# Kernel tuning notes

Hardware: AMD Instinct MI355X
Metric: run time of the kernel (lower is better)

## Reference

```python
import jax, jax.numpy as jnp
import numpy as np

B, CIN, COUT, N, M, K = 8, 128, 256, 8192, 2048, 16
BN_EPS = 1e-5


def setup_inputs() -> dict:
    key = jax.random.key(0)
    k1, k2, k3 = jax.random.split(key, 3)
    x = jax.random.normal(k1, (B, CIN, N), dtype=jnp.float32)
    coords = jax.random.normal(k2, (B, 3, N), dtype=jnp.float32)
    W = jax.random.normal(k3, (COUT, CIN), dtype=jnp.float32) * 0.05  # 1x1 conv, bias=False
    gamma = jnp.ones((COUT,), dtype=jnp.float32)   # BatchNorm2d weight
    beta = jnp.zeros((COUT,), dtype=jnp.float32)   # BatchNorm2d bias
    return {"x": x, "coords": coords, "W": W, "gamma": gamma, "beta": beta}


def furthest_point_sampling(coords, num_samples):
    """coords: (B,3,N) -> indices (B,num_samples) int32. Greedy FPS starting at index 0."""
    pts = coords.transpose(0, 2, 1)  # (B,N,3)
    b, n, _ = pts.shape
    idx0 = jnp.zeros((b,), dtype=jnp.int32)
    mind0 = jnp.full((b, n), 1e10, dtype=pts.dtype)

    def step(carry, _):
        mind, last = carry
        lastpt = jnp.take_along_axis(pts, last[:, None, None], axis=1)  # (b,1,3)
        d = jnp.sum((pts - lastpt) ** 2, axis=-1)                        # (b,n)
        mind = jnp.minimum(mind, d)
        nxt = jnp.argmax(mind, axis=-1).astype(jnp.int32)
        return (mind, nxt), nxt

    (_, _), rest = jax.lax.scan(step, (mind0, idx0), None, length=num_samples - 1)
    return jnp.concatenate([idx0[:, None], rest.T], axis=1)  # (b,num_samples)


def reference(x, coords, W, gamma, beta):
    b = x.shape[0]
    fps_idx = furthest_point_sampling(coords, M)                # (B,M)
    pts = coords.transpose(0, 2, 1)                             # (B,N,3)
    bidx = jnp.arange(b)[:, None]
    fps_pts = pts[bidx, fps_idx]                                # (B,M,3)

    # squared-distance matrix via ||a||^2 + ||b||^2 - 2ab (avoids (B,M,N,3) temp)
    d = (jnp.sum(fps_pts ** 2, -1)[:, :, None]
         + jnp.sum(pts ** 2, -1)[:, None, :]
         - 2.0 * jnp.einsum('bmd,bnd->bmn', fps_pts, pts))      # (B,M,N)
    _, knn_idx = jax.lax.top_k(-d, K)                           # (B,M,K) nearest (sorted)

    x_t = x.transpose(0, 2, 1)                                  # (B,N,Cin)
    knn = x_t[jnp.arange(b)[:, None, None], knn_idx]            # (B,M,K,Cin)

    # PointwiseConv2D: 1x1 conv (no bias) + BatchNorm2d (batch stats) + ReLU
    h = jnp.einsum('bmkc,oc->bmko', knn, W)                     # (B,M,K,Cout)
    mean = jnp.mean(h, axis=(0, 1, 2))
    var = jnp.var(h, axis=(0, 1, 2))
    h = (h - mean) * jax.lax.rsqrt(var + BN_EPS) * gamma + beta
    h = jax.nn.relu(h)

    y = jnp.max(h, axis=2).transpose(0, 2, 1)                   # (B,Cout,M), max over k
    fps_coords = fps_pts.transpose(0, 2, 1)                     # (B,3,M)
    return y, fps_coords
```

## Files before the change

kernel.cpp:

```cpp
#include <hip/hip_runtime.h>
#include <math.h>

#define B_ 8
#define CIN_ 128
#define COUT_ 256
#define N_ 8192
#define M_ 2048
#define K_ 16

__device__ __forceinline__ unsigned umax2(unsigned a, unsigned b) { return a > b ? a : b; }
__device__ __forceinline__ unsigned umin2(unsigned a, unsigned b) { return a < b ? a : b; }

__device__ __forceinline__ unsigned wave_reduce_umax(unsigned v) {
    v = umax2(v, (unsigned)__builtin_amdgcn_update_dpp(0, (int)v, 0x111, 0xf, 0xf, false));
    v = umax2(v, (unsigned)__builtin_amdgcn_update_dpp(0, (int)v, 0x112, 0xf, 0xf, false));
    v = umax2(v, (unsigned)__builtin_amdgcn_update_dpp(0, (int)v, 0x114, 0xf, 0xf, false));
    v = umax2(v, (unsigned)__builtin_amdgcn_update_dpp(0, (int)v, 0x118, 0xf, 0xf, false));
    v = umax2(v, (unsigned)__builtin_amdgcn_update_dpp(0, (int)v, 0x142, 0xf, 0xf, false));
    v = umax2(v, (unsigned)__builtin_amdgcn_update_dpp(0, (int)v, 0x143, 0xf, 0xf, false));
    return (unsigned)__builtin_amdgcn_readlane((int)v, 63);
}
__device__ __forceinline__ unsigned wave_reduce_umin(unsigned v) {
    v = umin2(v, (unsigned)__builtin_amdgcn_update_dpp(-1, (int)v, 0x111, 0xf, 0xf, false));
    v = umin2(v, (unsigned)__builtin_amdgcn_update_dpp(-1, (int)v, 0x112, 0xf, 0xf, false));
    v = umin2(v, (unsigned)__builtin_amdgcn_update_dpp(-1, (int)v, 0x114, 0xf, 0xf, false));
    v = umin2(v, (unsigned)__builtin_amdgcn_update_dpp(-1, (int)v, 0x118, 0xf, 0xf, false));
    v = umin2(v, (unsigned)__builtin_amdgcn_update_dpp(-1, (int)v, 0x142, 0xf, 0xf, false));
    v = umin2(v, (unsigned)__builtin_amdgcn_update_dpp(-1, (int)v, 0x143, 0xf, 0xf, false));
    return (unsigned)__builtin_amdgcn_readlane((int)v, 63);
}

__global__ __launch_bounds__(512) void fps_kernel(const float* __restrict__ coords,
                                                  float* __restrict__ fpts,
                                                  float* __restrict__ out_fps) {
#pragma clang fp contract(off)
    const int b = blockIdx.x;
    const int tid = threadIdx.x;
    const int lane = tid & 63;
    const int wid = tid >> 6;
    const float* cb = coords + (size_t)b * 3 * N_;

    __shared__ float4 pts[N_];
    __shared__ __align__(16) unsigned long long kbuf[2][8];
    __shared__ int wlist[M_];

    float px[16], py[16], pz[16], mind[16];
#pragma unroll
    for (int s = 0; s < 16; ++s) {
        int p = tid + s * 512;
        px[s] = cb[p];
        py[s] = cb[N_ + p];
        pz[s] = cb[2 * N_ + p];
        mind[s] = 1e10f;
        pts[p] = make_float4(px[s], py[s], pz[s], 0.f);
    }
    __syncthreads();
    float4 p0 = pts[0];
    float lx = p0.x, ly = p0.y, lz = p0.z;

    int par = 0;
    for (int m = 1; m < M_; ++m) {
        float bv = -1.0f; int bs = 0;
#pragma unroll
        for (int s = 0; s < 16; ++s) {
            float dx = px[s] - lx;
            float dy = py[s] - ly;
            float dz = pz[s] - lz;
            float d = __builtin_fmaf(dz, dz, __builtin_fmaf(dy, dy, dx * dx));
            float mn = fminf(mind[s], d);
            mind[s] = mn;
            if (mn > bv) { bv = mn; bs = s; }
        }
        int bi = tid + bs * 512;
        unsigned kd = __float_as_uint(bv);
        unsigned md = wave_reduce_umax(kd);
        unsigned cand = (kd == md) ? (unsigned)bi : 0xffffffffu;
        unsigned mi = wave_reduce_umin(cand);
        if (lane == 0)
            kbuf[par][wid] = ((unsigned long long)md << 32) |
                             (unsigned long long)(0xffffffffu - mi);
        __syncthreads();
        const unsigned long long* kb = kbuf[par];
        ulonglong2 q0 = *(const ulonglong2*)&kb[0];
        ulonglong2 q1 = *(const ulonglong2*)&kb[2];
        ulonglong2 q2 = *(const ulonglong2*)&kb[4];
        ulonglong2 q3 = *(const ulonglong2*)&kb[6];
        unsigned long long a0 = q0.x > q0.y ? q0.x : q0.y;
        unsigned long long a1 = q1.x > q1.y ? q1.x : q1.y;
        unsigned long long a2 = q2.x > q2.y ? q2.x : q2.y;
        unsigned long long a3 = q3.x > q3.y ? q3.x : q3.y;
        unsigned long long b01 = a0 > a1 ? a0 : a1;
        unsigned long long b23 = a2 > a3 ? a2 : a3;
        unsigned long long best = b01 > b23 ? b01 : b23;
        int widx = (int)(0xffffffffu - (unsigned)(best & 0xffffffffull));
        widx = ((unsigned)widx < (unsigned)N_) ? widx : 0;
        float4 wp = pts[widx];
        lx = wp.x; ly = wp.y; lz = wp.z;
        if (tid == 0) wlist[m] = widx;
        par ^= 1;
    }

    __syncthreads();
    for (int mm = tid; mm < M_; mm += 512) {
        int wi = (mm == 0) ? 0 : wlist[mm];
        wi = ((unsigned)wi < (unsigned)N_) ? wi : 0;
        float4 wp = pts[wi];
        ((float4*)fpts)[b * M_ + mm] = make_float4(wp.x, wp.y, wp.z, 0.f);
        out_fps[(size_t)b * 3 * M_ + 0 * M_ + mm] = wp.x;
        out_fps[(size_t)b * 3 * M_ + 1 * M_ + mm] = wp.y;
        out_fps[(size_t)b * 3 * M_ + 2 * M_ + mm] = wp.z;
    }
}

__global__ __launch_bounds__(256) void knn_kernel(const float* __restrict__ coords,
                                                  const float* __restrict__ fpts,
                                                  int* __restrict__ knn) {
#pragma clang fp contract(off)
    const int bidx = blockIdx.x;
    const int b = bidx >> 9;
    const int mg = bidx & 511;
    const int tid = threadIdx.x;
    const int lane = tid & 63;
    const int w = tid >> 6;
    const int m = mg * 4 + w;
    const int row = b * M_ + m;
    const float* cb = coords + (size_t)b * 3 * N_;

    __shared__ float4 tile[1024];

    float4 f = ((const float4*)fpts)[row];
    const float fx = f.x, fy = f.y, fz = f.z;
    const float sf = __builtin_fmaf(fz, fz, __builtin_fmaf(fy, fy, fx * fx));

    float ed = INFINITY; int ei = 0x7fffffff;
    float tau_d = INFINITY; int tau_i = 0x7fffffff;

    for (int t = 0; t < 8; ++t) {
        const int base = t * 1024;
#pragma unroll
        for (int j = 0; j < 4; ++j) {
            int idx = tid + 256 * j;
            int n = base + idx;
            float gx = cb[n], gy = cb[N_ + n], gz = cb[2 * N_ + n];
            float sp = __builtin_fmaf(gz, gz, __builtin_fmaf(gy, gy, gx * gx));
            tile[idx] = make_float4(gx, gy, gz, sp);
        }
        __syncthreads();
        for (int s = 0; s < 16; ++s) {
            int l = s * 64 + lane;
            float4 p = tile[l];
            int n = base + l;
            float dot = __builtin_fmaf(fz, p.z, __builtin_fmaf(fy, p.y, fx * p.x));
            float d = (sf + p.w) - 2.0f * dot;
            bool q = (d < tau_d) || (d == tau_d && n < tau_i);
            unsigned long long bal = __ballot(q);
            while (bal) {
                int lb = __ffsll(bal) - 1;
                bal &= bal - 1;
                float dv = __shfl(d, lb);
                int   iv = __shfl(n, lb);
                if ((dv < tau_d) || (dv == tau_d && iv < tau_i)) {
                    float pud = __shfl_up(ed, 1);
                    int   pui = __shfl_up(ei, 1);
                    bool cs = (dv < ed) || (dv == ed && iv < ei);
                    bool cp = (lane != 0) && ((dv < pud) || (dv == pud && iv < pui));
                    ed = cs ? (cp ? pud : dv) : ed;
                    ei = cs ? (cp ? pui : iv) : ei;
                    tau_d = __shfl(ed, 15);
                    tau_i = __shfl(ei, 15);
                }
            }
        }
        __syncthreads();
    }
    if (lane < K_) {
        int v = ei;
        knn[(size_t)row * K_ + lane] = ((unsigned)v < (unsigned)N_) ? v : 0;
    }
}

__global__ __launch_bounds__(256) void gemm_kernel(const float* __restrict__ x,
                                                   const float* __restrict__ W,
                                                   float* __restrict__ hp) {
    const int bid = blockIdx.x;
    const int b = bid >> 9;
    const int rem = bid & 511;
    const int n0 = (rem >> 2) * 64;
    const int o0 = (rem & 3) * 64;
    const int tid = threadIdx.x;
    const int tn = (tid & 15) * 4;
    const int to = (tid >> 4) * 4;
    const float* xg = x + (size_t)b * CIN_ * N_;

    __shared__ float Xs[64][64];
    __shared__ float Wt[64][68];

    float acc[4][4] = {};
    for (int kk = 0; kk < CIN_; kk += 64) {
#pragma unroll
        for (int i = 0; i < 16; ++i) {
            int e = tid + 256 * i;
            int r = e >> 6, q = e & 63;
            Xs[r][q] = xg[(size_t)(kk + r) * N_ + n0 + q];
            Wt[q][r] = W[(size_t)(o0 + r) * CIN_ + kk + q];
        }
        __syncthreads();
#pragma unroll 8
        for (int c = 0; c < 64; ++c) {
            float4 a = *(const float4*)&Xs[c][tn];
            float4 bb = *(const float4*)&Wt[c][to];
            float av[4] = {a.x, a.y, a.z, a.w};
            float bv[4] = {bb.x, bb.y, bb.z, bb.w};
#pragma unroll
            for (int j = 0; j < 4; ++j)
#pragma unroll
                for (int l = 0; l < 4; ++l)
                    acc[j][l] += av[j] * bv[l];
        }
        __syncthreads();
    }
#pragma unroll
    for (int j = 0; j < 4; ++j) {
        float4 v = make_float4(acc[j][0], acc[j][1], acc[j][2], acc[j][3]);
        *(float4*)&hp[((size_t)b * N_ + n0 + tn + j) * COUT_ + o0 + to] = v;
    }
}

__global__ __launch_bounds__(256) void stats_partial_kernel(const float* __restrict__ hp,
                                                            const int* __restrict__ knn,
                                                            double* __restrict__ partial,
                                                            double* __restrict__ partial2) {
    const int o = threadIdx.x;
    const int g0 = blockIdx.x * 1024;
    double s = 0.0, s2 = 0.0;
    for (int r = 0; r < 1024; ++r) {
        int g = g0 + r;
        int row = g >> 4;
        int k = g & 15;
        int b = row >> 11;
        int n = knn[row * K_ + k];
        n = ((unsigned)n < (unsigned)N_) ? n : 0;
        double h = (double)hp[((size_t)b * N_ + n) * COUT_ + o];
        s += h;
        s2 += h * h;
    }
    partial[(size_t)blockIdx.x * 256 + o] = s;
    partial2[(size_t)blockIdx.x * 256 + o] = s2;
}

__global__ void bn_final_kernel(const double* __restrict__ partial,
                                const double* __restrict__ partial2,
                                const float* __restrict__ gamma,
                                const float* __restrict__ beta,
                                float* __restrict__ scale,
                                float* __restrict__ bias) {
    int o = threadIdx.x;
    double s = 0.0, s2 = 0.0;
    for (int j = 0; j < 256; ++j) {
        s += partial[(size_t)j * 256 + o];
        s2 += partial2[(size_t)j * 256 + o];
    }
    const double inv = 1.0 / (double)(B_ * M_ * K_);
    double mean = s * inv;
    double var = s2 * inv - mean * mean;
    if (var < 0.0) var = 0.0;
    double r = 1.0 / sqrt(var + 1e-5);
    double g = (double)gamma[o];
    scale[o] = (float)(r * g);
    bias[o] = (float)((double)beta[o] - mean * r * g);
}

__global__ __launch_bounds__(256) void finalize_kernel(const float* __restrict__ hp,
                                                       const int* __restrict__ knn,
                                                       const float* __restrict__ scale,
                                                       const float* __restrict__ bias,
                                                       float* __restrict__ y) {
    const int b = blockIdx.x >> 6;
    const int m0 = (blockIdx.x & 63) * 32;
    const int tid = threadIdx.x;
    __shared__ int kidx[512];
    __shared__ float tile[32][257];

    for (int e = tid; e < 512; e += 256) {
        int n = knn[(b * M_ + m0 + (e >> 4)) * K_ + (e & 15)];
        kidx[e] = ((unsigned)n < (unsigned)N_) ? n : 0;
    }
    __syncthreads();

    const float s = scale[tid];
    const float t = bias[tid];
    const float* hb = hp + (size_t)b * N_ * COUT_;
    for (int mm = 0; mm < 32; ++mm) {
        float v = -INFINITY;
#pragma unroll
        for (int k = 0; k < K_; ++k) {
            int n = kidx[mm * 16 + k];
            float h = hb[(size_t)n * COUT_ + tid];
            v = fmaxf(v, h * s + t);
        }
        v = fmaxf(v, 0.0f);
        tile[mm][tid] = v;
    }
    __syncthreads();
#pragma unroll
    for (int r = 0; r < 32; ++r) {
        int o2 = r * 8 + (tid >> 5);
        int mm = tid & 31;
        y[((size_t)b * COUT_ + o2) * M_ + m0 + mm] = tile[mm][o2];
    }
}

__global__ void sentinel_kernel(float* out, float v) { out[0] = v; }

extern "C" void kernel_launch(void* const* d_in, const int* in_sizes, int n_in,
                              void* d_out, int out_size, void* d_ws, size_t ws_size,
                              hipStream_t stream) {
    const float* x = (const float*)d_in[0];
    const float* coords = (const float*)d_in[1];
    const float* W = (const float*)d_in[2];
    const float* gamma = (const float*)d_in[3];
    const float* beta = (const float*)d_in[4];
    float* y = (float*)d_out;
    float* out_fps = y + (size_t)B_ * COUT_ * M_;

    if (n_in != 5 ||
        in_sizes[0] != B_ * CIN_ * N_ ||
        in_sizes[1] != B_ * 3 * N_ ||
        in_sizes[2] != COUT_ * CIN_ ||
        in_sizes[3] != COUT_ || in_sizes[4] != COUT_ ||
        out_size != B_ * COUT_ * M_ + B_ * 3 * M_) {
        sentinel_kernel<<<1, 1, 0, stream>>>(y, -2.0e6f);
        return;
    }

    const size_t HP_BYTES = (size_t)B_ * N_ * COUT_ * 4;
    const size_t FPTS_BYTES = (size_t)B_ * M_ * 16;
    const size_t KNN_BYTES = (size_t)B_ * M_ * K_ * 4;
    const size_t PART_BYTES = (size_t)256 * 256 * 8;
    const size_t NEED = HP_BYTES + FPTS_BYTES + KNN_BYTES + 2 * PART_BYTES + 8192;
    if (ws_size < NEED) {
        sentinel_kernel<<<1, 1, 0, stream>>>(y, -1.0e6f);
        return;
    }
    char* ws = (char*)d_ws;
    float* hp = (float*)ws;
    float* fpts = (float*)(ws + HP_BYTES);
    int* knn = (int*)(ws + HP_BYTES + FPTS_BYTES);
    double* partial = (double*)(ws + HP_BYTES + FPTS_BYTES + KNN_BYTES);
    double* partial2 = (double*)(ws + HP_BYTES + FPTS_BYTES + KNN_BYTES + PART_BYTES);
    float* scale = (float*)(ws + HP_BYTES + FPTS_BYTES + KNN_BYTES + 2 * PART_BYTES);
    float* bias = scale + 256;

    fps_kernel<<<B_, 512, 0, stream>>>(coords, fpts, out_fps);
    knn_kernel<<<B_ * 512, 256, 0, stream>>>(coords, fpts, knn);
    gemm_kernel<<<B_ * 512, 256, 0, stream>>>(x, W, hp);
    stats_partial_kernel<<<256, 256, 0, stream>>>(hp, knn, partial, partial2);
    bn_final_kernel<<<1, 256, 0, stream>>>(partial, partial2, gamma, beta, scale, bias);
    finalize_kernel<<<512, 256, 0, stream>>>(hp, knn, scale, bias, y);
}
```

Baseline: 1.954 ms.

## Shrink FPS block to 256 threads and fuse argmax into a single 64-bit DPP reduction

The FPS kernel now runs 256 threads, each holding 32 points in registers instead of 16, so each barrier-synchronised iteration involves 4 waves instead of 8. The two-pass wave reduction (max of the distance, then min of the index) is replaced by one DPP reduction on a packed (distance, inverted index) 64-bit key, which shortens the serial critical path of each of the 2047 steps. The cost is twice the per-thread serial distance work and higher register pressure (launch_bounds 256,1).

```diff
diff --git a/kernel.cpp b/kernel.cpp
--- a/kernel.cpp
+++ b/kernel.cpp
@@ -8,31 +8,16 @@
 #define M_ 2048
 #define K_ 16
 
-__device__ __forceinline__ unsigned umax2(unsigned a, unsigned b) { return a > b ? a : b; }
-__device__ __forceinline__ unsigned umin2(unsigned a, unsigned b) { return a < b ? a : b; }
-
-__device__ __forceinline__ unsigned wave_reduce_umax(unsigned v) {
-    v = umax2(v, (unsigned)__builtin_amdgcn_update_dpp(0, (int)v, 0x111, 0xf, 0xf, false));
-    v = umax2(v, (unsigned)__builtin_amdgcn_update_dpp(0, (int)v, 0x112, 0xf, 0xf, false));
-    v = umax2(v, (unsigned)__builtin_amdgcn_update_dpp(0, (int)v, 0x114, 0xf, 0xf, false));
-    v = umax2(v, (unsigned)__builtin_amdgcn_update_dpp(0, (int)v, 0x118, 0xf, 0xf, false));
-    v = umax2(v, (unsigned)__builtin_amdgcn_update_dpp(0, (int)v, 0x142, 0xf, 0xf, false));
-    v = umax2(v, (unsigned)__builtin_amdgcn_update_dpp(0, (int)v, 0x143, 0xf, 0xf, false));
-    return (unsigned)__builtin_amdgcn_readlane((int)v, 63);
-}
-__device__ __forceinline__ unsigned wave_reduce_umin(unsigned v) {
-    v = umin2(v, (unsigned)__builtin_amdgcn_update_dpp(-1, (int)v, 0x111, 0xf, 0xf, false));
-    v = umin2(v, (unsigned)__builtin_amdgcn_update_dpp(-1, (int)v, 0x112, 0xf, 0xf, false));
-    v = umin2(v, (unsigned)__builtin_amdgcn_update_dpp(-1, (int)v, 0x114, 0xf, 0xf, false));
-    v = umin2(v, (unsigned)__builtin_amdgcn_update_dpp(-1, (int)v, 0x118, 0xf, 0xf, false));
-    v = umin2(v, (unsigned)__builtin_amdgcn_update_dpp(-1, (int)v, 0x142, 0xf, 0xf, false));
-    v = umin2(v, (unsigned)__builtin_amdgcn_update_dpp(-1, (int)v, 0x143, 0xf, 0xf, false));
-    return (unsigned)__builtin_amdgcn_readlane((int)v, 63);
-}
-
-__global__ __launch_bounds__(512) void fps_kernel(const float* __restrict__ coords,
-                                                  float* __restrict__ fpts,
-                                                  float* __restrict__ out_fps) {
+#define KSTEP(CTL) {                                                                     \
+    unsigned h2 = (unsigned)__builtin_amdgcn_update_dpp(0, (int)hi, CTL, 0xf, 0xf, false); \
+    unsigned l2 = (unsigned)__builtin_amdgcn_update_dpp(0, (int)lo, CTL, 0xf, 0xf, false); \
+    unsigned long long cur = ((unsigned long long)hi << 32) | lo;                        \
+    unsigned long long oth = ((unsigned long long)h2 << 32) | l2;                        \
+    if (oth > cur) { hi = h2; lo = l2; } }
+
+__global__ __launch_bounds__(256, 1) void fps_kernel(const float* __restrict__ coords,
+                                                     float* __restrict__ fpts,
+                                                     float* __restrict__ out_fps) {
 #pragma clang fp contract(off)
     const int b = blockIdx.x;
     const int tid = threadIdx.x;
@@ -41,13 +26,13 @@
     const float* cb = coords + (size_t)b * 3 * N_;
 
     __shared__ float4 pts[N_];
-    __shared__ __align__(16) unsigned long long kbuf[2][8];
+    __shared__ __align__(16) unsigned long long kbuf[2][4];
     __shared__ int wlist[M_];
 
-    float px[16], py[16], pz[16], mind[16];
-#pragma unroll
-    for (int s = 0; s < 16; ++s) {
-        int p = tid + s * 512;
+    float px[32], py[32], pz[32], mind[32];
+#pragma unroll
+    for (int s = 0; s < 32; ++s) {
+        int p = tid + s * 256;
         px[s] = cb[p];
         py[s] = cb[N_ + p];
         pz[s] = cb[2 * N_ + p];
@@ -62,7 +47,7 @@
     for (int m = 1; m < M_; ++m) {
         float bv = -1.0f; int bs = 0;
 #pragma unroll
-        for (int s = 0; s < 16; ++s) {
+        for (int s = 0; s < 32; ++s) {
             float dx = px[s] - lx;
             float dy = py[s] - ly;
             float dz = pz[s] - lz;
@@ -71,27 +56,22 @@
             mind[s] = mn;
             if (mn > bv) { bv = mn; bs = s; }
         }
-        int bi = tid + bs * 512;
-        unsigned kd = __float_as_uint(bv);
-        unsigned md = wave_reduce_umax(kd);
-        unsigned cand = (kd == md) ? (unsigned)bi : 0xffffffffu;
-        unsigned mi = wave_reduce_umin(cand);
-        if (lane == 0)
-            kbuf[par][wid] = ((unsigned long long)md << 32) |
-                             (unsigned long long)(0xffffffffu - mi);
-        __syncthreads();
-        const unsigned long long* kb = kbuf[par];
-        ulonglong2 q0 = *(const ulonglong2*)&kb[0];
-        ulonglong2 q1 = *(const ulonglong2*)&kb[2];
-        ulonglong2 q2 = *(const ulonglong2*)&kb[4];
-        ulonglong2 q3 = *(const ulonglong2*)&kb[6];
+        unsigned hi = __float_as_uint(bv);
+        unsigned lo = 0xffffffffu - (unsigned)(tid + bs * 256);
+        KSTEP(0x111)
+        KSTEP(0x112)
+        KSTEP(0x114)
+        KSTEP(0x118)
+        KSTEP(0x142)
+        KSTEP(0x143)
+        if (lane == 63)
+            kbuf[par][wid] = ((unsigned long long)hi << 32) | (unsigned long long)lo;
+        __syncthreads();
+        ulonglong2 q0 = *(const ulonglong2*)&kbuf[par][0];
+        ulonglong2 q1 = *(const ulonglong2*)&kbuf[par][2];
         unsigned long long a0 = q0.x > q0.y ? q0.x : q0.y;
         unsigned long long a1 = q1.x > q1.y ? q1.x : q1.y;
-        unsigned long long a2 = q2.x > q2.y ? q2.x : q2.y;
-        unsigned long long a3 = q3.x > q3.y ? q3.x : q3.y;
-        unsigned long long b01 = a0 > a1 ? a0 : a1;
-        unsigned long long b23 = a2 > a3 ? a2 : a3;
-        unsigned long long best = b01 > b23 ? b01 : b23;
+        unsigned long long best = a0 > a1 ? a0 : a1;
         int widx = (int)(0xffffffffu - (unsigned)(best & 0xffffffffull));
         widx = ((unsigned)widx < (unsigned)N_) ? widx : 0;
         float4 wp = pts[widx];
@@ -101,7 +81,7 @@
     }
 
     __syncthreads();
-    for (int mm = tid; mm < M_; mm += 512) {
+    for (int mm = tid; mm < M_; mm += 256) {
         int wi = (mm == 0) ? 0 : wlist[mm];
         wi = ((unsigned)wi < (unsigned)N_) ? wi : 0;
         float4 wp = pts[wi];
@@ -351,7 +331,7 @@
     float* scale = (float*)(ws + HP_BYTES + FPTS_BYTES + KNN_BYTES + 2 * PART_BYTES);
     float* bias = scale + 256;
 
-    fps_kernel<<<B_, 512, 0, stream>>>(coords, fpts, out_fps);
+    fps_kernel<<<B_, 256, 0, stream>>>(coords, fpts, out_fps);
     knn_kernel<<<B_ * 512, 256, 0, stream>>>(coords, fpts, knn);
     gemm_kernel<<<B_ * 512, 256, 0, stream>>>(x, W, hp);
     stats_partial_kernel<<<256, 256, 0, stream>>>(hp, knn, partial, partial2);
```

Result: slower. 2.325 ms (+19.0%).

## Fuse FPS and pointwise GEMM into one launch so GEMM overlaps FPS

Applied to the files above, without the earlier changes.

FPS and the input GEMM now run in a single kernel. The first 8 blocks do the serial furthest-point sampling, and the remaining 2048 blocks compute the GEMM with 512-thread, 128-wide tiles. Shared memory is a union of the two layouts. The goal is to hide the GEMM inside the long, low-occupancy FPS phase, which runs on only 8 blocks. In exchange, every block reserves the large FPS shared-memory footprint, which limits GEMM occupancy, and the GEMM tile shape changes.

```diff
diff --git a/kernel.cpp b/kernel.cpp
--- a/kernel.cpp
+++ b/kernel.cpp
@@ -7,6 +7,8 @@
 #define N_ 8192
 #define M_ 2048
 #define K_ 16
+
+#define GEMM_BLOCKS 2048
 
 __device__ __forceinline__ unsigned umax2(unsigned a, unsigned b) { return a > b ? a : b; }
 __device__ __forceinline__ unsigned umin2(unsigned a, unsigned b) { return a < b ? a : b; }
@@ -30,85 +32,148 @@
     return (unsigned)__builtin_amdgcn_readlane((int)v, 63);
 }
 
-__global__ __launch_bounds__(512) void fps_kernel(const float* __restrict__ coords,
-                                                  float* __restrict__ fpts,
-                                                  float* __restrict__ out_fps) {
+__global__ __launch_bounds__(512) void fps_gemm_kernel(const float* __restrict__ coords,
+                                                       const float* __restrict__ x,
+                                                       const float* __restrict__ W,
+                                                       float* __restrict__ fpts,
+                                                       float* __restrict__ out_fps,
+                                                       float* __restrict__ hp) {
+    __shared__ union {
+        struct {
+            float4 pts[N_];
+            unsigned long long kbuf[2][8];
+            int wlist[M_];
+        } f;
+        struct {
+            float Xs[64][128];
+            float Wt[64][68];
+        } g;
+    } sm;
+
+    const int tid = threadIdx.x;
+
+    if (blockIdx.x < B_) {
 #pragma clang fp contract(off)
-    const int b = blockIdx.x;
-    const int tid = threadIdx.x;
-    const int lane = tid & 63;
-    const int wid = tid >> 6;
-    const float* cb = coords + (size_t)b * 3 * N_;
-
-    __shared__ float4 pts[N_];
-    __shared__ __align__(16) unsigned long long kbuf[2][8];
-    __shared__ int wlist[M_];
-
-    float px[16], py[16], pz[16], mind[16];
-#pragma unroll
-    for (int s = 0; s < 16; ++s) {
-        int p = tid + s * 512;
-        px[s] = cb[p];
-        py[s] = cb[N_ + p];
-        pz[s] = cb[2 * N_ + p];
-        mind[s] = 1e10f;
-        pts[p] = make_float4(px[s], py[s], pz[s], 0.f);
-    }
-    __syncthreads();
-    float4 p0 = pts[0];
-    float lx = p0.x, ly = p0.y, lz = p0.z;
-
-    int par = 0;
-    for (int m = 1; m < M_; ++m) {
-        float bv = -1.0f; int bs = 0;
+        const int b = blockIdx.x;
+        const int lane = tid & 63;
+        const int wid = tid >> 6;
+        const float* cb = coords + (size_t)b * 3 * N_;
+        float4* pts = sm.f.pts;
+        unsigned long long (*kbuf)[8] = sm.f.kbuf;
+        int* wlist = sm.f.wlist;
+
+        float px[16], py[16], pz[16], mind[16];
 #pragma unroll
         for (int s = 0; s < 16; ++s) {
-            float dx = px[s] - lx;
-            float dy = py[s] - ly;
-            float dz = pz[s] - lz;
-            float d = __builtin_fmaf(dz, dz, __builtin_fmaf(dy, dy, dx * dx));
-            float mn = fminf(mind[s], d);
-            mind[s] = mn;
-            if (mn > bv) { bv = mn; bs = s; }
-        }
-        int bi = tid + bs * 512;
-        unsigned kd = __float_as_uint(bv);
-        unsigned md = wave_reduce_umax(kd);
-        unsigned cand = (kd == md) ? (unsigned)bi : 0xffffffffu;
-        unsigned mi = wave_reduce_umin(cand);
-        if (lane == 0)
-            kbuf[par][wid] = ((unsigned long long)md << 32) |
-                             (unsigned long long)(0xffffffffu - mi);
+            int p = tid + s * 512;
+            px[s] = cb[p];
+            py[s] = cb[N_ + p];
+            pz[s] = cb[2 * N_ + p];
+            mind[s] = 1e10f;
+            pts[p] = make_float4(px[s], py[s], pz[s], 0.f);
+        }
         __syncthreads();
-        const unsigned long long* kb = kbuf[par];
-        ulonglong2 q0 = *(const ulonglong2*)&kb[0];
-        ulonglong2 q1 = *(const ulonglong2*)&kb[2];
-        ulonglong2 q2 = *(const ulonglong2*)&kb[4];
-        ulonglong2 q3 = *(const ulonglong2*)&kb[6];
-        unsigned long long a0 = q0.x > q0.y ? q0.x : q0.y;
-        unsigned long long a1 = q1.x > q1.y ? q1.x : q1.y;
-        unsigned long long a2 = q2.x > q2.y ? q2.x : q2.y;
-        unsigned long long a3 = q3.x > q3.y ? q3.x : q3.y;
-        unsigned long long b01 = a0 > a1 ? a0 : a1;
-        unsigned long long b23 = a2 > a3 ? a2 : a3;
-        unsigned long long best = b01 > b23 ? b01 : b23;
-        int widx = (int)(0xffffffffu - (unsigned)(best & 0xffffffffull));
-        widx = ((unsigned)widx < (unsigned)N_) ? widx : 0;
-        float4 wp = pts[widx];
-        lx = wp.x; ly = wp.y; lz = wp.z;
-        if (tid == 0) wlist[m] = widx;
-        par ^= 1;
-    }
-
-    __syncthreads();
-    for (int mm = tid; mm < M_; mm += 512) {
-        int wi = (mm == 0) ? 0 : wlist[mm];
-        wi = ((unsigned)wi < (unsigned)N_) ? wi : 0;
-        float4 wp = pts[wi];
-        ((float4*)fpts)[b * M_ + mm] = make_float4(wp.x, wp.y, wp.z, 0.f);
-        out_fps[(size_t)b * 3 * M_ + 0 * M_ + mm] = wp.x;
-        out_fps[(size_t)b * 3 * M_ + 1 * M_ + mm] = wp.y;
-        out_fps[(size_t)b * 3 * M_ + 2 * M_ + mm] = wp.z;
+        float4 p0 = pts[0];
+        float lx = p0.x, ly = p0.y, lz = p0.z;
+
+        int par = 0;
+        for (int m = 1; m < M_; ++m) {
+            float bv = -1.0f; int bs = 0;
+#pragma unroll
+            for (int s = 0; s < 16; ++s) {
+                float dx = px[s] - lx;
+                float dy = py[s] - ly;
+                float dz = pz[s] - lz;
+                float d = __builtin_fmaf(dz, dz, __builtin_fmaf(dy, dy, dx * dx));
+                float mn = fminf(mind[s], d);
+                mind[s] = mn;
+                if (mn > bv) { bv = mn; bs = s; }
+            }
+            int bi = tid + bs * 512;
+            unsigned kd = __float_as_uint(bv);
+            unsigned md = wave_reduce_umax(kd);
+            unsigned cand = (kd == md) ? (unsigned)bi : 0xffffffffu;
+            unsigned mi = wave_reduce_umin(cand);
+            if (lane == 0)
+                kbuf[par][wid] = ((unsigned long long)md << 32) |
+                                 (unsigned long long)(0xffffffffu - mi);
+            __syncthreads();
+            const unsigned long long* kb = kbuf[par];
+            ulonglong2 q0 = *(const ulonglong2*)&kb[0];
+            ulonglong2 q1 = *(const ulonglong2*)&kb[2];
+            ulonglong2 q2 = *(const ulonglong2*)&kb[4];
+            ulonglong2 q3 = *(const ulonglong2*)&kb[6];
+            unsigned long long a0 = q0.x > q0.y ? q0.x : q0.y;
+            unsigned long long a1 = q1.x > q1.y ? q1.x : q1.y;
+            unsigned long long a2 = q2.x > q2.y ? q2.x : q2.y;
+            unsigned long long a3 = q3.x > q3.y ? q3.x : q3.y;
+            unsigned long long b01 = a0 > a1 ? a0 : a1;
+            unsigned long long b23 = a2 > a3 ? a2 : a3;
+            unsigned long long best = b01 > b23 ? b01 : b23;
+            int widx = (int)(0xffffffffu - (unsigned)(best & 0xffffffffull));
+            widx = ((unsigned)widx < (unsigned)N_) ? widx : 0;
+            float4 wp = pts[widx];
+            lx = wp.x; ly = wp.y; lz = wp.z;
+            if (tid == 0) wlist[m] = widx;
+            par ^= 1;
+        }
+
+        __syncthreads();
+        for (int mm = tid; mm < M_; mm += 512) {
+            int wi = (mm == 0) ? 0 : wlist[mm];
+            wi = ((unsigned)wi < (unsigned)N_) ? wi : 0;
+            float4 wp = pts[wi];
+            ((float4*)fpts)[b * M_ + mm] = make_float4(wp.x, wp.y, wp.z, 0.f);
+            out_fps[(size_t)b * 3 * M_ + 0 * M_ + mm] = wp.x;
+            out_fps[(size_t)b * 3 * M_ + 1 * M_ + mm] = wp.y;
+            out_fps[(size_t)b * 3 * M_ + 2 * M_ + mm] = wp.z;
+        }
+    } else {
+        const int gb = blockIdx.x - B_;
+        const int b = gb >> 8;
+        const int rem = gb & 255;
+        const int n0 = (rem >> 2) * 128;
+        const int o0 = (rem & 3) * 64;
+        const int tn = (tid & 31) * 4;
+        const int to = (tid >> 5) * 4;
+        const float* xg = x + (size_t)b * CIN_ * N_;
+        float (*Xs)[128] = sm.g.Xs;
+        float (*Wt)[68] = sm.g.Wt;
+
+        float acc[4][4] = {};
+        for (int kk = 0; kk < CIN_; kk += 64) {
+#pragma unroll
+            for (int i = 0; i < 16; ++i) {
+                int e = tid + 512 * i;
+                int r = e >> 7, q = e & 127;
+                Xs[r][q] = xg[(size_t)(kk + r) * N_ + n0 + q];
+            }
+#pragma unroll
+            for (int i = 0; i < 8; ++i) {
+                int e = tid + 512 * i;
+                int r = e >> 6, q = e & 63;
+                Wt[q][r] = W[(size_t)(o0 + r) * CIN_ + kk + q];
+            }
+            __syncthreads();
+#pragma unroll 8
+            for (int c = 0; c < 64; ++c) {
+                float4 a = *(const float4*)&Xs[c][tn];
+                float4 bb = *(const float4*)&Wt[c][to];
+                float av[4] = {a.x, a.y, a.z, a.w};
+                float bv[4] = {bb.x, bb.y, bb.z, bb.w};
+#pragma unroll
+                for (int j = 0; j < 4; ++j)
+#pragma unroll
+                    for (int l = 0; l < 4; ++l)
+                        acc[j][l] += av[j] * bv[l];
+            }
+            __syncthreads();
+        }
+#pragma unroll
+        for (int j = 0; j < 4; ++j) {
+            float4 v = make_float4(acc[j][0], acc[j][1], acc[j][2], acc[j][3]);
+            *(float4*)&hp[((size_t)b * N_ + n0 + tn + j) * COUT_ + o0 + to] = v;
+        }
     }
 }
 
@@ -179,53 +244,6 @@
     }
 }
 
-__global__ __launch_bounds__(256) void gemm_kernel(const float* __restrict__ x,
-                                                   const float* __restrict__ W,
-                                                   float* __restrict__ hp) {
-    const int bid = blockIdx.x;
-    const int b = bid >> 9;
-    const int rem = bid & 511;
-    const int n0 = (rem >> 2) * 64;
-    const int o0 = (rem & 3) * 64;
-    const int tid = threadIdx.x;
-    const int tn = (tid & 15) * 4;
-    const int to = (tid >> 4) * 4;
-    const float* xg = x + (size_t)b * CIN_ * N_;
-
-    __shared__ float Xs[64][64];
-    __shared__ float Wt[64][68];
-
-    float acc[4][4] = {};
-    for (int kk = 0; kk < CIN_; kk += 64) {
-#pragma unroll
-        for (int i = 0; i < 16; ++i) {
-            int e = tid + 256 * i;
-            int r = e >> 6, q = e & 63;
-            Xs[r][q] = xg[(size_t)(kk + r) * N_ + n0 + q];
-            Wt[q][r] = W[(size_t)(o0 + r) * CIN_ + kk + q];
-        }
-        __syncthreads();
-#pragma unroll 8
-        for (int c = 0; c < 64; ++c) {
-            float4 a = *(const float4*)&Xs[c][tn];
-            float4 bb = *(const float4*)&Wt[c][to];
-            float av[4] = {a.x, a.y, a.z, a.w};
-            float bv[4] = {bb.x, bb.y, bb.z, bb.w};
-#pragma unroll
-            for (int j = 0; j < 4; ++j)
-#pragma unroll
-                for (int l = 0; l < 4; ++l)
-                    acc[j][l] += av[j] * bv[l];
-        }
-        __syncthreads();
-    }
-#pragma unroll
-    for (int j = 0; j < 4; ++j) {
-        float4 v = make_float4(acc[j][0], acc[j][1], acc[j][2], acc[j][3]);
-        *(float4*)&hp[((size_t)b * N_ + n0 + tn + j) * COUT_ + o0 + to] = v;
-    }
-}
-
 __global__ __launch_bounds__(256) void stats_partial_kernel(const float* __restrict__ hp,
                                                             const int* __restrict__ knn,
                                                             double* __restrict__ partial,
@@ -351,9 +369,8 @@
     float* scale = (float*)(ws + HP_BYTES + FPTS_BYTES + KNN_BYTES + 2 * PART_BYTES);
     float* bias = scale + 256;
 
-    fps_kernel<<<B_, 512, 0, stream>>>(coords, fpts, out_fps);
+    fps_gemm_kernel<<<B_ + GEMM_BLOCKS, 512, 0, stream>>>(coords, x, W, fpts, out_fps, hp);
     knn_kernel<<<B_ * 512, 256, 0, stream>>>(coords, fpts, knn);
-    gemm_kernel<<<B_ * 512, 256, 0, stream>>>(x, W, hp);
     stats_partial_kernel<<<256, 256, 0, stream>>>(hp, knn, partial, partial2);
     bn_final_kernel<<<1, 256, 0, stream>>>(partial, partial2, gamma, beta, scale, bias);
     finalize_kernel<<<512, 256, 0, stream>>>(hp, knn, scale, bias, y);
```

Result: faster. 1.896 ms (-3.0%).
